# Optimization experiments

Hardware: AMD Instinct MI355X
Metric: run time of the kernel (lower is better)

The kernel has to match this reference:

```python
import jax, jax.numpy as jnp
import numpy as np

N_NODES = 50000
N_EDGES = 600000
D_FEAT = 128


def setup_inputs() -> dict:
    key = jax.random.key(0)
    k_h, k_src, k_dst, k_dt, k_norm = jax.random.split(key, 5)
    h = jax.random.normal(k_h, (N_NODES, D_FEAT), dtype=jnp.float32)
    src = jax.random.randint(k_src, (N_EDGES,), 0, N_NODES, dtype=jnp.int32)
    dst = jax.random.randint(k_dst, (N_EDGES,), 0, N_NODES, dtype=jnp.int32)
    # dt: non-negative time deltas (scaled up a bit so the decay matters)
    dt = jax.random.uniform(k_dt, (N_EDGES,), dtype=jnp.float32) * 10.0
    # norm: symmetric-normalization-like positive edge weights
    norm = jax.random.uniform(k_norm, (N_EDGES,), dtype=jnp.float32)
    decay_lam = jnp.full((1,), 0.1, dtype=jnp.float32)  # nn.Parameter(0.1)
    return {"h": h, "src": src, "dst": dst, "dt": dt, "norm": norm, "decay_lam": decay_lam}


def reference(h, src, dst, dt, norm, decay_lam):
    # lam = relu(decay_lam) + 1e-4  (scalar)
    lam = jax.nn.relu(decay_lam[0]) + 1e-4
    # per-edge temporal weight: norm * exp(-lam * dt)   [E]
    w = norm * jnp.exp(-lam * dt)
    # u_mul_e: gather source features, scale by edge weight  [E, D]
    m = h[src] * w[:, None]
    # sum-reduce messages at destination nodes  [N, D]
    h_new = jax.ops.segment_sum(m, dst, num_segments=h.shape[0])
    return h_new
```

## Files before the change

kernel.cpp:

```cpp
#include <hip/hip_runtime.h>
#include <hip/hip_bf16.h>

#define D_FEAT 128
#define BIN_SHIFT 7
#define NODES_PER_BIN 128
#define BCAP 4096
#define EPB 4096
#define T1 512
#define CSR_L_CAP 5120
#define OVF_CAP 4096

typedef float f2v __attribute__((ext_vector_type(2)));

__device__ __forceinline__ unsigned bf16_rne(float f) {
    unsigned u = __float_as_uint(f);
    return (u + 0x7fffu + ((u >> 16) & 1u)) >> 16;
}

__global__ void __launch_bounds__(T1)
conv_bin_kernel(const float* __restrict__ h,
                const int* __restrict__ src, const int* __restrict__ dst,
                const float* __restrict__ dt, const float* __restrict__ norm,
                const float* __restrict__ decay_lam,
                unsigned* __restrict__ hb,
                int* __restrict__ bin_cursor, unsigned long long* __restrict__ binned,
                int* __restrict__ ovf_cnt, int* __restrict__ ovf_d,
                int* __restrict__ ovf_s, float* __restrict__ ovf_w,
                int E, int HN4, int convBlocks, int NB) {
    __shared__ unsigned hist[T1];
    __shared__ unsigned tmp[T1];
    __shared__ unsigned cur[T1];
    __shared__ unsigned gbase[T1];
    __shared__ unsigned long long stage[EPB];
    __shared__ unsigned gaddr[EPB];

    int t = threadIdx.x;
    if (blockIdx.x < convBlocks) {
        int i = blockIdx.x * T1 + t;
        if (i < HN4) {
            float4 v = ((const float4*)h)[i];
            ((uint2*)hb)[i] = make_uint2(bf16_rne(v.x) | (bf16_rne(v.y) << 16),
                                         bf16_rne(v.z) | (bf16_rne(v.w) << 16));
        }
        return;
    }

    int e0 = (blockIdx.x - convBlocks) * EPB;
    int cnt_blk = min(EPB, E - e0);

    hist[t] = 0; cur[t] = 0; gbase[t] = 0;
    __syncthreads();

    float lam = fmaxf(decay_lam[0], 0.0f) + 1e-4f;

    unsigned long long ent[EPB / T1];
    int bn[EPB / T1];
    #pragma unroll
    for (int k = 0; k < EPB / T1; ++k) {
        int e = e0 + k * T1 + t;
        bn[k] = -1;
        if (e < E) {
            int s = src[e], d = dst[e];
            float w = norm[e] * expf(-lam * dt[e]);
            int b = d >> BIN_SHIFT;
            int l = d & (NODES_PER_BIN - 1);
            ent[k] = ((unsigned long long)l << 32) | (((unsigned)s << 16) | bf16_rne(w));
            bn[k] = b;
            atomicAdd(&hist[b], 1u);
        }
    }
    __syncthreads();
    tmp[t] = hist[t];
    __syncthreads();
    for (int off = 1; off < T1; off <<= 1) {
        unsigned v = (t >= off) ? tmp[t - off] : 0;
        __syncthreads();
        tmp[t] += v;
        __syncthreads();
    }
    unsigned base_t = tmp[t] - hist[t];
    if (t < NB && hist[t] > 0)
        gbase[t] = (unsigned)atomicAdd(&bin_cursor[t], (int)hist[t]);
    __syncthreads();
    tmp[t] = base_t;
    __syncthreads();

    #pragma unroll
    for (int k = 0; k < EPB / T1; ++k) {
        if (bn[k] >= 0) {
            int b = bn[k];
            unsigned loc = atomicAdd(&cur[b], 1u);
            unsigned p = tmp[b] + loc;
            unsigned gp = gbase[b] + loc;
            stage[p] = ent[k];
            if (gp < BCAP) {
                gaddr[p] = (unsigned)b * BCAP + gp;
            } else {
                gaddr[p] = 0xFFFFFFFFu;
                int o = atomicAdd(ovf_cnt, 1);
                if (o < OVF_CAP) {
                    int l = (int)(ent[k] >> 32);
                    ovf_d[o] = (b << BIN_SHIFT) | l;
                    ovf_s[o] = (int)((ent[k] >> 16) & 0xFFFFu);
                    ovf_w[o] = __uint_as_float(((unsigned)ent[k] & 0xFFFFu) << 16);
                }
            }
        }
    }
    __syncthreads();
    #pragma unroll
    for (int k = 0; k < EPB / T1; ++k) {
        int idx = k * T1 + t;
        if (idx < cnt_blk) {
            unsigned g = gaddr[idx];
            if (g != 0xFFFFFFFFu) binned[g] = stage[idx];
        }
    }
}

__global__ void __launch_bounds__(T1)
sort_gather_kernel(const unsigned long long* __restrict__ binned,
                   const int* __restrict__ bin_cursor,
                   const unsigned* __restrict__ hb,
                   const int* __restrict__ ovf_cnt, const int* __restrict__ ovf_d,
                   const int* __restrict__ ovf_s, const float* __restrict__ ovf_w,
                   float* __restrict__ out, int N) {
    __shared__ unsigned hist[NODES_PER_BIN];
    __shared__ unsigned padoff[NODES_PER_BIN];
    __shared__ unsigned cur[NODES_PER_BIN];
    __shared__ unsigned csr_l[CSR_L_CAP];

    int b = blockIdx.x;
    int t = threadIdx.x;
    int cnt = min(bin_cursor[b], BCAP);

    if (t < NODES_PER_BIN) { hist[t] = 0; cur[t] = 0; }
    for (int i = t; i < CSR_L_CAP; i += T1) csr_l[i] = 0;
    __syncthreads();

    unsigned long long ent[BCAP / T1];
    size_t base_in = (size_t)b * BCAP;
    #pragma unroll
    for (int k = 0; k < BCAP / T1; ++k) {
        int idx = k * T1 + t;
        ent[k] = ~0ull;
        if (idx < cnt) {
            unsigned long long e = binned[base_in + idx];
            ent[k] = e;
            atomicAdd(&hist[(int)(e >> 32)], 1u);
        }
    }
    __syncthreads();

    unsigned pc = 0;
    if (t < NODES_PER_BIN) { pc = (hist[t] + 7u) & ~7u; padoff[t] = pc; }
    __syncthreads();
    for (int off = 1; off < NODES_PER_BIN; off <<= 1) {
        unsigned v = 0;
        if (t < NODES_PER_BIN && t >= off) v = padoff[t - off];
        __syncthreads();
        if (t < NODES_PER_BIN) padoff[t] += v;
        __syncthreads();
    }
    if (t < NODES_PER_BIN) padoff[t] -= pc;
    __syncthreads();

    #pragma unroll
    for (int k = 0; k < BCAP / T1; ++k) {
        if (ent[k] != ~0ull) {
            int l = (int)(ent[k] >> 32);
            unsigned p = padoff[l] + atomicAdd(&cur[l], 1u);
            csr_l[p] = (unsigned)ent[k];
        }
    }
    __syncthreads();

    int wid = t >> 6;
    int lane = t & 63;
    int nodes = min(NODES_PER_BIN, N - (b << BIN_SHIFT));
    bool ovf_bin = bin_cursor[b] > BCAP;

    for (int l = wid; l < nodes; l += 8) {
        unsigned base = padoff[l];
        unsigned mr = (hist[l] + 7u) & ~7u;
        float accx = 0.0f, accy = 0.0f;
        for (unsigned j = 0; j < mr; j += 8) {
            unsigned u0 = csr_l[base + j + 0];
            unsigned u1 = csr_l[base + j + 1];
            unsigned u2 = csr_l[base + j + 2];
            unsigned u3 = csr_l[base + j + 3];
            unsigned u4 = csr_l[base + j + 4];
            unsigned u5 = csr_l[base + j + 5];
            unsigned u6 = csr_l[base + j + 6];
            unsigned u7 = csr_l[base + j + 7];
            unsigned v0 = hb[(size_t)(u0 >> 16) * 64 + lane];
            unsigned v1 = hb[(size_t)(u1 >> 16) * 64 + lane];
            unsigned v2 = hb[(size_t)(u2 >> 16) * 64 + lane];
            unsigned v3 = hb[(size_t)(u3 >> 16) * 64 + lane];
            unsigned v4 = hb[(size_t)(u4 >> 16) * 64 + lane];
            unsigned v5 = hb[(size_t)(u5 >> 16) * 64 + lane];
            unsigned v6 = hb[(size_t)(u6 >> 16) * 64 + lane];
            unsigned v7 = hb[(size_t)(u7 >> 16) * 64 + lane];
            #define ACC(u, v)                                             \
            {   float wf = __uint_as_float((u) << 16);                    \
                float vx = __uint_as_float((v) << 16);                    \
                float vy = __uint_as_float((v) & 0xffff0000u);            \
                accx += vx * wf; accy += vy * wf; }
            ACC(u0, v0) ACC(u1, v1) ACC(u2, v2) ACC(u3, v3)
            ACC(u4, v4) ACC(u5, v5) ACC(u6, v6) ACC(u7, v7)
            #undef ACC
        }
        int node = (b << BIN_SHIFT) + l;
        if (ovf_bin) {
            int oc = min(*ovf_cnt, OVF_CAP);
            for (int o = 0; o < oc; ++o) {
                if (ovf_d[o] == node) {
                    float we = ovf_w[o];
                    unsigned v = hb[(size_t)ovf_s[o] * 64 + lane];
                    accx += __uint_as_float(v << 16) * we;
                    accy += __uint_as_float(v & 0xffff0000u) * we;
                }
            }
        }
        f2v r;
        r.x = accx; r.y = accy;
        __builtin_nontemporal_store(r, (f2v*)(out + (size_t)node * D_FEAT) + lane);
    }
}


__global__ void degree_kernel(const int* __restrict__ dst, int* __restrict__ deg, int E) {
    int e = blockIdx.x * blockDim.x + threadIdx.x;
    if (e >= E) return;
    atomicAdd(&deg[dst[e]], 1);
}

__global__ void scan_blocks(const int* __restrict__ deg, int* __restrict__ offs,
                            int* __restrict__ blockSums, int N) {
    __shared__ int tmp[256];
    int tid = threadIdx.x;
    int gid = blockIdx.x * 256 + tid;
    int v = (gid < N) ? deg[gid] : 0;
    tmp[tid] = v;
    __syncthreads();
    for (int off = 1; off < 256; off <<= 1) {
        int t = (tid >= off) ? tmp[tid - off] : 0;
        __syncthreads();
        tmp[tid] += t;
        __syncthreads();
    }
    if (gid < N) offs[gid] = tmp[tid] - v;
    if (tid == 255) blockSums[blockIdx.x] = tmp[255];
}

__global__ void scan_sums(int* __restrict__ blockSums, int* __restrict__ blockOffs, int nb) {
    __shared__ int tmp[256];
    int tid = threadIdx.x;
    int v = (tid < nb) ? blockSums[tid] : 0;
    tmp[tid] = v;
    __syncthreads();
    for (int off = 1; off < 256; off <<= 1) {
        int t = (tid >= off) ? tmp[tid - off] : 0;
        __syncthreads();
        tmp[tid] += t;
        __syncthreads();
    }
    if (tid < nb) blockOffs[tid] = tmp[tid] - v;
}

__global__ void scan_fixup(int* __restrict__ offs, const int* __restrict__ blockOffs,
                           int* __restrict__ cursor, int N) {
    int gid = blockIdx.x * 256 + threadIdx.x;
    if (gid >= N) return;
    int o = offs[gid] + blockOffs[blockIdx.x];
    offs[gid] = o;
    cursor[gid] = o;
}

__global__ void bucket_kernel(const int* __restrict__ src, const int* __restrict__ dst,
                              const float* __restrict__ dt, const float* __restrict__ norm,
                              const float* __restrict__ decay_lam,
                              int* __restrict__ cursor, float2* __restrict__ pairs, int E) {
    int e = blockIdx.x * blockDim.x + threadIdx.x;
    if (e >= E) return;
    float lam = fmaxf(decay_lam[0], 0.0f) + 1e-4f;
    float w = norm[e] * expf(-lam * dt[e]);
    int d = dst[e];
    int pos = atomicAdd(&cursor[d], 1);
    float2 p;
    p.x = __int_as_float(src[e]);
    p.y = w;
    pairs[pos] = p;
}

__global__ void __launch_bounds__(256)
gather_kernel(const float* __restrict__ h,
              const int* __restrict__ offs, const int* __restrict__ deg,
              const float2* __restrict__ pairs, float* __restrict__ out, int N) {
    int node = blockIdx.x * 4 + (threadIdx.x >> 6);
    if (node >= N) return;
    int lane = threadIdx.x & 63;
    int start = offs[node];
    int end = start + deg[node];
    float accx = 0.0f, accy = 0.0f;
    for (int j = start; j < end; ++j) {
        float2 p = pairs[j];
        int s = __float_as_int(p.x);
        float we = p.y;
        float2 v = ((const float2*)(h + (size_t)s * D_FEAT))[lane];
        accx += v.x * we;
        accy += v.y * we;
    }
    float2 r; r.x = accx; r.y = accy;
    ((float2*)(out + (size_t)node * D_FEAT))[lane] = r;
}

extern "C" void kernel_launch(void* const* d_in, const int* in_sizes, int n_in,
                              void* d_out, int out_size, void* d_ws, size_t ws_size,
                              hipStream_t stream) {
    const float* h         = (const float*)d_in[0];
    const int*   src       = (const int*)d_in[1];
    const int*   dst       = (const int*)d_in[2];
    const float* dt        = (const float*)d_in[3];
    const float* norm      = (const float*)d_in[4];
    const float* decay_lam = (const float*)d_in[5];
    float* out = (float*)d_out;

    const int E  = in_sizes[1];
    const int HN = in_sizes[0];
    const int N  = out_size / D_FEAT;
    const int NB = (N + NODES_PER_BIN - 1) >> BIN_SHIFT;

    auto align64 = [](size_t x) { return (x + 63) & ~(size_t)63; };
    size_t sz_binc = align64((size_t)NB * 4);
    size_t sz_ovfc = 64;
    size_t sz_ovf  = align64((size_t)OVF_CAP * 4);
    size_t sz_binn = align64((size_t)NB * BCAP * 8);
    size_t sz_hb   = align64((size_t)HN * 2);
    size_t need = sz_binc + sz_ovfc + 3 * sz_ovf + sz_binn + sz_hb;

    if (ws_size >= need && N <= 65536 && (HN & 3) == 0 && NB <= T1) {
        char* ws = (char*)d_ws;
        int* bin_cursor = (int*)ws;                 ws += sz_binc;
        int* ovf_cnt    = (int*)ws;                 ws += sz_ovfc;
        int* ovf_d      = (int*)ws;                 ws += sz_ovf;
        int* ovf_s      = (int*)ws;                 ws += sz_ovf;
        float* ovf_w    = (float*)ws;               ws += sz_ovf;
        unsigned long long* binned = (unsigned long long*)ws;  ws += sz_binn;
        unsigned* hb    = (unsigned*)ws;

        hipMemsetAsync(bin_cursor, 0, sz_binc + sz_ovfc, stream);

        const int HN4 = HN / 4;
        const int convBlocks = (HN4 + T1 - 1) / T1;
        const int binBlocks  = (E + EPB - 1) / EPB;
        conv_bin_kernel<<<convBlocks + binBlocks, T1, 0, stream>>>(
            h, src, dst, dt, norm, decay_lam, hb, bin_cursor, binned,
            ovf_cnt, ovf_d, ovf_s, ovf_w, E, HN4, convBlocks, NB);

        sort_gather_kernel<<<NB, T1, 0, stream>>>(
            binned, bin_cursor, hb, ovf_cnt, ovf_d, ovf_s, ovf_w, out, N);
    } else {
        const int nb = (N + 255) / 256;
        char* ws = (char*)d_ws;
        int*    dega      = (int*)ws;     ws += (size_t)N * 4;
        int*    offsa     = (int*)ws;     ws += (size_t)N * 4;
        int*    cursor    = (int*)ws;     ws += (size_t)N * 4;
        int*    blockSums = (int*)ws;     ws += 256 * 4;
        int*    blockOffs = (int*)ws;     ws += 256 * 4;
        float2* pairs     = (float2*)ws;

        hipMemsetAsync(dega, 0, (size_t)N * 4, stream);
        degree_kernel<<<(E + 255) / 256, 256, 0, stream>>>(dst, dega, E);
        scan_blocks<<<nb, 256, 0, stream>>>(dega, offsa, blockSums, N);
        scan_sums<<<1, 256, 0, stream>>>(blockSums, blockOffs, nb);
        scan_fixup<<<nb, 256, 0, stream>>>(offsa, blockOffs, cursor, N);
        bucket_kernel<<<(E + 255) / 256, 256, 0, stream>>>(
            src, dst, dt, norm, decay_lam, cursor, pairs, E);
        gather_kernel<<<(N + 3) / 4, 256, 0, stream>>>(h, offsa, dega, pairs, out, N);
    }
}
```

Measured before the change: 127.8 us.

## Scatter binned edges directly and use wavefront shuffle scan for node offsets

Result: no change. 127.2 us (-0.5%).

```diff
diff --git a/kernel.cpp b/kernel.cpp
--- a/kernel.cpp
+++ b/kernel.cpp
@@ -5,7 +5,7 @@
 #define BIN_SHIFT 7
 #define NODES_PER_BIN 128
 #define BCAP 4096
-#define EPB 4096
+#define EPB 2048
 #define T1 512
 #define CSR_L_CAP 5120
 #define OVF_CAP 4096
@@ -28,11 +28,8 @@
                 int* __restrict__ ovf_s, float* __restrict__ ovf_w,
                 int E, int HN4, int convBlocks, int NB) {
     __shared__ unsigned hist[T1];
-    __shared__ unsigned tmp[T1];
     __shared__ unsigned cur[T1];
     __shared__ unsigned gbase[T1];
-    __shared__ unsigned long long stage[EPB];
-    __shared__ unsigned gaddr[EPB];
 
     int t = threadIdx.x;
     if (blockIdx.x < convBlocks) {
@@ -46,9 +43,8 @@
     }
 
     int e0 = (blockIdx.x - convBlocks) * EPB;
-    int cnt_blk = min(EPB, E - e0);
-
-    hist[t] = 0; cur[t] = 0; gbase[t] = 0;
+
+    hist[t] = 0; cur[t] = 0;
     __syncthreads();
 
     float lam = fmaxf(decay_lam[0], 0.0f) + 1e-4f;
@@ -70,33 +66,19 @@
         }
     }
     __syncthreads();
-    tmp[t] = hist[t];
-    __syncthreads();
-    for (int off = 1; off < T1; off <<= 1) {
-        unsigned v = (t >= off) ? tmp[t - off] : 0;
-        __syncthreads();
-        tmp[t] += v;
-        __syncthreads();
-    }
-    unsigned base_t = tmp[t] - hist[t];
+
     if (t < NB && hist[t] > 0)
         gbase[t] = (unsigned)atomicAdd(&bin_cursor[t], (int)hist[t]);
-    __syncthreads();
-    tmp[t] = base_t;
     __syncthreads();
 
     #pragma unroll
     for (int k = 0; k < EPB / T1; ++k) {
         if (bn[k] >= 0) {
             int b = bn[k];
-            unsigned loc = atomicAdd(&cur[b], 1u);
-            unsigned p = tmp[b] + loc;
-            unsigned gp = gbase[b] + loc;
-            stage[p] = ent[k];
+            unsigned gp = gbase[b] + atomicAdd(&cur[b], 1u);
             if (gp < BCAP) {
-                gaddr[p] = (unsigned)b * BCAP + gp;
+                binned[(size_t)b * BCAP + gp] = ent[k];
             } else {
-                gaddr[p] = 0xFFFFFFFFu;
                 int o = atomicAdd(ovf_cnt, 1);
                 if (o < OVF_CAP) {
                     int l = (int)(ent[k] >> 32);
@@ -105,15 +87,6 @@
                     ovf_w[o] = __uint_as_float(((unsigned)ent[k] & 0xFFFFu) << 16);
                 }
             }
-        }
-    }
-    __syncthreads();
-    #pragma unroll
-    for (int k = 0; k < EPB / T1; ++k) {
-        int idx = k * T1 + t;
-        if (idx < cnt_blk) {
-            unsigned g = gaddr[idx];
-            if (g != 0xFFFFFFFFu) binned[g] = stage[idx];
         }
     }
 }
@@ -129,6 +102,7 @@
     __shared__ unsigned padoff[NODES_PER_BIN];
     __shared__ unsigned cur[NODES_PER_BIN];
     __shared__ unsigned csr_l[CSR_L_CAP];
+    __shared__ unsigned wtot;
 
     int b = blockIdx.x;
     int t = threadIdx.x;
@@ -152,17 +126,17 @@
     }
     __syncthreads();
 
-    unsigned pc = 0;
-    if (t < NODES_PER_BIN) { pc = (hist[t] + 7u) & ~7u; padoff[t] = pc; }
-    __syncthreads();
-    for (int off = 1; off < NODES_PER_BIN; off <<= 1) {
-        unsigned v = 0;
-        if (t < NODES_PER_BIN && t >= off) v = padoff[t - off];
-        __syncthreads();
-        if (t < NODES_PER_BIN) padoff[t] += v;
-        __syncthreads();
-    }
-    if (t < NODES_PER_BIN) padoff[t] -= pc;
+    unsigned pc = 0, val = 0;
+    if (t < NODES_PER_BIN) { pc = (hist[t] + 7u) & ~7u; val = pc; }
+    #pragma unroll
+    for (int off = 1; off < 64; off <<= 1) {
+        unsigned u = __shfl_up(val, off, 64);
+        if ((t & 63) >= off) val += u;
+    }
+    if (t == 63) wtot = val;
+    __syncthreads();
+    if (t < NODES_PER_BIN)
+        padoff[t] = val + ((t >= 64) ? wtot : 0u) - pc;
     __syncthreads();
 
     #pragma unroll
```
